# Performance work log

Hardware: AMD Instinct MI355X
Metric: run time of the kernel (lower is better)

Reference implementation:

```python
import jax, jax.numpy as jnp
import numpy as np

N_HEAD = 16


def setup_inputs() -> dict:
    key = jax.random.key(0)
    ks = jax.random.split(key, 4)
    B, S, NX = 2, 2048, 1024
    x = jax.random.normal(ks[0], (B, S, NX), dtype=jnp.float32)
    # additive causal mask: 0 where j <= i, -1e9 where j > i
    causal = jnp.tril(jnp.ones((S, S), dtype=jnp.float32))
    attention_mask = ((1.0 - causal) * -1e9)[None, None, :, :]
    w_attn = jax.random.normal(ks[1], (NX, 3 * NX), dtype=jnp.float32) * 0.02
    b_attn = jnp.zeros((3 * NX,), dtype=jnp.float32)
    w_proj = jax.random.normal(ks[2], (NX, NX), dtype=jnp.float32) * 0.02
    b_proj = jnp.zeros((NX,), dtype=jnp.float32)
    return {"x": x, "attention_mask": attention_mask, "w_attn": w_attn,
            "b_attn": b_attn, "w_proj": w_proj, "b_proj": b_proj}


def reference(x, attention_mask, w_attn, b_attn, w_proj, b_proj):
    B, S, NX = x.shape
    H = N_HEAD
    D = NX // H
    # c_attn (Conv1D): x @ W + b -> [B, S, 3*NX]
    qkv = jnp.einsum('bse,ef->bsf', x, w_attn) + b_attn
    q, k, v = jnp.split(qkv, 3, axis=-1)
    # split heads -> [B, H, S, D]
    q = q.reshape(B, S, H, D).transpose(0, 2, 1, 3)
    k = k.reshape(B, S, H, D).transpose(0, 2, 1, 3)
    v = v.reshape(B, S, H, D).transpose(0, 2, 1, 3)
    # scores [B, H, S, S], scaled by 1/sqrt(head_dim) since scale=True
    w = jnp.einsum('bhqd,bhkd->bhqk', q, k) / jnp.sqrt(jnp.float32(D))
    w = w + attention_mask
    w = jax.nn.softmax(w, axis=-1)
    # attn_dropout is identity in eval / p=0
    a = jnp.einsum('bhqk,bhkd->bhqd', w, v)
    # merge heads -> [B, S, NX]
    a = a.transpose(0, 2, 1, 3).reshape(B, S, NX)
    # c_proj (Conv1D)
    out = jnp.einsum('bse,ef->bsf', a, w_proj) + b_proj
    # resid_dropout identity
    return out
```

## Files before the change

### kernel.cpp

```cpp
#include <hip/hip_runtime.h>
#include <hip/hip_bf16.h>

typedef __bf16 bf16;
typedef __bf16 bf16x8 __attribute__((ext_vector_type(8)));
typedef __bf16 bf16x4 __attribute__((ext_vector_type(4)));
typedef float  f32x4  __attribute__((ext_vector_type(4)));
typedef float  f32x16 __attribute__((ext_vector_type(16)));

#define MFMA16(A,B,C) __builtin_amdgcn_mfma_f32_16x16x32_bf16(A,B,C,0,0,0)
#define MFMA32(A,B,C) __builtin_amdgcn_mfma_f32_32x32x16_bf16(A,B,C,0,0,0)
#define EXP2(x) __builtin_amdgcn_exp2f(x)

static constexpr int SEQ = 2048;
static constexpr int NXC = 1024;
#define QSCALE 0.1803368801111244f

static __device__ inline unsigned packb(float lo, float hi) {
  union { bf16 h[2]; unsigned u; } x;
  x.h[0] = (bf16)lo; x.h[1] = (bf16)hi;
  return x.u;
}
static __device__ inline bf16x8 frag_from_words(unsigned a, unsigned b,
                                                unsigned c, unsigned d) {
  union { unsigned u[4]; bf16x8 v; } x;
  x.u[0] = a; x.u[1] = b; x.u[2] = c; x.u[3] = d;
  return x.v;
}
__device__ __forceinline__ void gload16(const bf16* g, bf16* l) {
  __builtin_amdgcn_global_load_lds(
      (const __attribute__((address_space(1))) void*)g,
      (__attribute__((address_space(3))) void*)l, 16, 0, 0);
}

__global__ __launch_bounds__(256) void f2b_kernel(const float* __restrict__ in,
                                                  bf16* __restrict__ out, int n4) {
  int i = blockIdx.x * blockDim.x + threadIdx.x;
  if (i < n4) {
    float4 v = ((const float4*)in)[i];
    bf16x4 o;
    o[0] = (bf16)v.x; o[1] = (bf16)v.y; o[2] = (bf16)v.z; o[3] = (bf16)v.w;
    ((bf16x4*)out)[i] = o;
  }
}

__global__ __launch_bounds__(256) void tr_f2b(const float* __restrict__ in,
                                              bf16* __restrict__ out, int R, int C) {
  __shared__ bf16 t[64][72];
  const int c0 = blockIdx.x * 64, r0 = blockIdx.y * 64;
  const int tid = threadIdx.x;
  const int lr = tid >> 4, lc = (tid & 15) * 4;
  #pragma unroll
  for (int p = 0; p < 4; ++p) {
    int rr = lr + p * 16;
    float4 v = *(const float4*)&in[(size_t)(r0 + rr) * C + c0 + lc];
    t[lc + 0][rr] = (bf16)v.x; t[lc + 1][rr] = (bf16)v.y;
    t[lc + 2][rr] = (bf16)v.z; t[lc + 3][rr] = (bf16)v.w;
  }
  __syncthreads();
  const int orow = tid >> 3, ocol = (tid & 7) * 8;
  #pragma unroll
  for (int p = 0; p < 2; ++p) {
    int rr = orow + p * 32;
    *(bf16x8*)&out[(size_t)(c0 + rr) * R + r0 + ocol] = *(const bf16x8*)&t[rr][ocol];
  }
}

template<int MODE>
__global__ __launch_bounds__(256) void gemm_bt(
    const bf16* __restrict__ A, const bf16* __restrict__ BT,
    const float* __restrict__ bias,
    bf16* __restrict__ qb, bf16* __restrict__ kb, bf16* __restrict__ vtb,
    float* __restrict__ outf, int K, int N)
{
  __shared__ bf16 As[128 * 32];
  __shared__ bf16 Bs[128 * 32];

  const int tid  = threadIdx.x;
  const int lane = tid & 63;
  const int w    = tid >> 6;
  const int m0   = blockIdx.y * 128;
  const int n0   = blockIdx.x * 128;
  const int wrow = (w >> 1) * 64;
  const int wcol = (w & 1) * 64;
  const int g    = lane >> 4;
  const int c16  = lane & 15;

  f32x4 acc[4][4];
  #pragma unroll
  for (int i = 0; i < 4; ++i)
    #pragma unroll
    for (int j = 0; j < 4; ++j)
      acc[i][j] = f32x4{0.f, 0.f, 0.f, 0.f};

  const bf16* gA = A  + (size_t)(m0 + w * 16 + (lane >> 2)) * K + (lane & 3) * 8;
  const bf16* gB = BT + (size_t)(n0 + w * 16 + (lane >> 2)) * K + (lane & 3) * 8;
  bf16* lA = As + (w * 16) * 32;
  bf16* lB = Bs + (w * 16) * 32;
  const size_t rstep = (size_t)64 * K;

  for (int k0 = 0; k0 < K; k0 += 32) {
    gload16(gA + k0,         lA);
    gload16(gA + k0 + rstep, lA + 64 * 32);
    gload16(gB + k0,         lB);
    gload16(gB + k0 + rstep, lB + 64 * 32);
    __syncthreads();

    bf16x8 af[4], bfr[4];
    #pragma unroll
    for (int i = 0; i < 4; ++i)
      af[i] = *(const bf16x8*)&As[(wrow + i * 16 + c16) * 32 + g * 8];
    #pragma unroll
    for (int j = 0; j < 4; ++j)
      bfr[j] = *(const bf16x8*)&Bs[(wcol + j * 16 + c16) * 32 + g * 8];
    #pragma unroll
    for (int i = 0; i < 4; ++i)
      #pragma unroll
      for (int j = 0; j < 4; ++j)
        acc[i][j] = MFMA16(af[i], bfr[j], acc[i][j]);
    __syncthreads();
  }

  #pragma unroll
  for (int i = 0; i < 4; ++i) {
    #pragma unroll
    for (int j = 0; j < 4; ++j) {
      #pragma unroll
      for (int r = 0; r < 4; ++r) {
        int gm = m0 + wrow + i * 16 + g * 4 + r;
        int gn = n0 + wcol + j * 16 + c16;
        float v = acc[i][j][r] + bias[gn];
        if (MODE == 0) {
          int which = gn >> 10;
          int cc = gn & 1023;
          int hh = cc >> 6, dd = cc & 63;
          int bb = gm >> 11, ss = gm & 2047;
          int bh = bb * 16 + hh;
          if (which == 0)
            qb[((size_t)bh * SEQ + ss) * 64 + dd] = (bf16)(v * QSCALE);
          else if (which == 1)
            kb[((size_t)bh * SEQ + ss) * 64 + dd] = (bf16)v;
          else
            vtb[((size_t)bh * 64 + dd) * SEQ + ss] = (bf16)v;
        } else {
          outf[(size_t)gm * N + gn] = v;
        }
      }
    }
  }
}

__global__ __launch_bounds__(256, 2) void attn7_kernel(
    const bf16* __restrict__ q, const bf16* __restrict__ k,
    const bf16* __restrict__ vt, bf16* __restrict__ aout)
{
  __shared__ bf16 smem[2][8192];

  const int tid  = threadIdx.x;
  const int lane = tid & 63;
  const int w    = tid >> 6;
  const int hi   = lane >> 5;
  const int q_l  = lane & 31;
  const int bid  = blockIdx.x;
  const int bh   = bid & 31;
  const int strip= 15 - (bid >> 5);
  const int qr0  = strip * 128 + w * 32;
  const int qg   = qr0 + q_l;
  const int nt   = 2 * strip + 2;

  bf16x8 qf[4];
  {
    const bf16* qp = q + ((size_t)bh * SEQ + qr0 + q_l) * 64 + hi * 8;
    #pragma unroll
    for (int c = 0; c < 4; ++c) qf[c] = *(const bf16x8*)(qp + c * 16);
  }

  f32x16 Ot0 = (f32x16)0.f, Ot1 = (f32x16)0.f;
  float mrun = -INFINITY, lrun = 0.f;

  const int r1 = tid >> 3;
  const int c1 = (tid & 7) ^ (r1 & 7);
  const bf16* kB = k  + (size_t)bh * SEQ * 64;
  const bf16* vB = vt + (size_t)bh * 64 * SEQ;
  const int sw = q_l & 7;

  auto STAGE = [&](int b, int kv0) {
    bf16* buf = &smem[b][0];
    gload16(kB + (size_t)(kv0 + r1) * 64 + c1 * 8,       buf + w * 512);
    gload16(kB + (size_t)(kv0 + r1 + 32) * 64 + c1 * 8,  buf + 2048 + w * 512);
    gload16(vB + (size_t)r1 * SEQ + kv0 + c1 * 8,        buf + 4096 + w * 512);
    gload16(vB + (size_t)(r1 + 32) * SEQ + kv0 + c1 * 8, buf + 6144 + w * 512);
  };

  auto do_tile = [&](int b, int kv0) {
    const bf16* Kb = &smem[b][0];
    const bf16* Vb = &smem[b][4096];

    bf16x8 kf[8];
    #pragma unroll
    for (int c = 0; c < 4; ++c) {
      int ch = ((2 * c + hi) ^ sw) * 8;
      kf[c]     = *(const bf16x8*)&Kb[q_l * 64 + ch];
      kf[4 + c] = *(const bf16x8*)&Kb[(q_l + 32) * 64 + ch];
    }

    f32x16 st0 = (f32x16)0.f, st1 = (f32x16)0.f;
    __builtin_amdgcn_s_setprio(1);
    #pragma unroll
    for (int c = 0; c < 4; ++c) {
      st0 = MFMA32(kf[c],     qf[c], st0);
      st1 = MFMA32(kf[4 + c], qf[c], st1);
    }
    __builtin_amdgcn_s_setprio(0);

    bf16x8 vf[8];
    #pragma unroll
    for (int t2 = 0; t2 < 2; ++t2)
      #pragma unroll
      for (int h = 0; h < 2; ++h) {
        int ch = ((4 * t2 + 2 * h + hi) ^ sw) * 8;
        vf[t2 * 2 + h]     = *(const bf16x8*)&Vb[q_l * 64 + ch];
        vf[4 + t2 * 2 + h] = *(const bf16x8*)&Vb[(q_l + 32) * 64 + ch];
      }

    if (kv0 + 63 > qr0) {
      #pragma unroll
      for (int r = 0; r < 16; ++r) {
        int kvl = kv0 + (r & 3) + 8 * (r >> 2) + 4 * hi;
        if (kvl > qg)      st0[r] = -1e30f;
        if (kvl + 32 > qg) st1[r] = -1e30f;
      }
    }

    float m8[8];
    #pragma unroll
    for (int r = 0; r < 8; ++r)
      m8[r] = fmaxf(fmaxf(st0[r], st0[r + 8]), fmaxf(st1[r], st1[r + 8]));
    #pragma unroll
    for (int r = 0; r < 4; ++r) m8[r] = fmaxf(m8[r], m8[r + 4]);
    float pmax = fmaxf(fmaxf(m8[0], m8[1]), fmaxf(m8[2], m8[3]));

    float mnew;
    if (__all(pmax <= mrun + 8.f)) {
      mnew = mrun;
    } else {
      float pm = fmaxf(pmax, __shfl_xor(pmax, 32));
      mnew = fmaxf(mrun, pm);
      const float sc = EXP2(mrun - mnew);
      lrun *= sc;
      Ot0 *= sc;
      Ot1 *= sc;
      mrun = mnew;
    }

    #pragma unroll
    for (int r = 0; r < 16; ++r) {
      st0[r] = EXP2(st0[r] - mnew);
      st1[r] = EXP2(st1[r] - mnew);
    }

    float s8[8];
    #pragma unroll
    for (int r = 0; r < 8; ++r)
      s8[r] = (st0[r] + st0[r + 8]) + (st1[r] + st1[r + 8]);
    #pragma unroll
    for (int r = 0; r < 4; ++r) s8[r] += s8[r + 4];
    lrun += (s8[0] + s8[1]) + (s8[2] + s8[3]);

    unsigned pw[16];
    #pragma unroll
    for (int m = 0; m < 8; ++m) {
      pw[m]     = packb(st0[2 * m], st0[2 * m + 1]);
      pw[8 + m] = packb(st1[2 * m], st1[2 * m + 1]);
    }
    __builtin_amdgcn_s_setprio(1);
    #pragma unroll
    for (int t2 = 0; t2 < 2; ++t2) {
      #pragma unroll
      for (int h = 0; h < 2; ++h) {
        auto sa = __builtin_amdgcn_permlane32_swap((int)pw[t2 * 8 + 4 * h + 0],
                                                   (int)pw[t2 * 8 + 4 * h + 2], false, false);
        auto sb = __builtin_amdgcn_permlane32_swap((int)pw[t2 * 8 + 4 * h + 1],
                                                   (int)pw[t2 * 8 + 4 * h + 3], false, false);
        bf16x8 pb = frag_from_words((unsigned)sa[0], (unsigned)sb[0],
                                    (unsigned)sa[1], (unsigned)sb[1]);
        Ot0 = MFMA32(vf[t2 * 2 + h],     pb, Ot0);
        Ot1 = MFMA32(vf[4 + t2 * 2 + h], pb, Ot1);
      }
    }
    __builtin_amdgcn_s_setprio(0);
  };

  STAGE(0, 0);
  asm volatile("s_waitcnt vmcnt(0)" ::: "memory");
  __builtin_amdgcn_s_barrier();

  int cur = 0;
  for (int t = 0; t < nt - 1; ++t) {
    STAGE(cur ^ 1, (t + 1) << 6);
    if ((t << 6) <= qr0 + 31) do_tile(cur, t << 6);
    asm volatile("s_waitcnt vmcnt(0)" ::: "memory");
    __builtin_amdgcn_s_barrier();
    cur ^= 1;
  }
  do_tile(cur, (nt - 1) << 6);


  lrun += __shfl_xor(lrun, 32);
  const float inv = 1.f / lrun;

  __syncthreads();
  bf16* ot = &smem[0][0];
  const int orow = w * 32 + q_l;
  #pragma unroll
  for (int r = 0; r < 16; ++r) {
    int d = (r & 3) + 8 * (r >> 2) + 4 * hi;
    ot[orow * 72 + d]      = (bf16)(Ot0[r] * inv);
    ot[orow * 72 + d + 32] = (bf16)(Ot1[r] * inv);
  }
  __syncthreads();

  const int bb = bh >> 4, hh = bh & 15;
  const int qrow = w * 32 + (lane >> 1), half = lane & 1;
  const bf16* src = ot + qrow * 72 + half * 32;
  bf16* dst = aout + ((size_t)bb * SEQ + strip * 128 + qrow) * NXC + hh * 64 + half * 32;
  #pragma unroll
  for (int e = 0; e < 4; ++e)
    *(bf16x8*)(dst + e * 8) = *(const bf16x8*)(src + e * 8);
}

extern "C" void kernel_launch(void* const* d_in, const int* in_sizes, int n_in,
                              void* d_out, int out_size, void* d_ws, size_t ws_size,
                              hipStream_t stream) {
  const float* x      = (const float*)d_in[0];
  const float* w_attn = (const float*)d_in[2];
  const float* b_attn = (const float*)d_in[3];
  const float* w_proj = (const float*)d_in[4];
  const float* b_proj = (const float*)d_in[5];
  float* out = (float*)d_out;

  char* p = (char*)d_ws;
  bf16* xb   = (bf16*)p; p += (size_t)4194304 * 2;
  bf16* wabT = (bf16*)p; p += (size_t)3145728 * 2;
  bf16* wpbT = (bf16*)p; p += (size_t)1048576 * 2;
  bf16* qb   = (bf16*)p; p += (size_t)4194304 * 2;
  bf16* kb   = (bf16*)p; p += (size_t)4194304 * 2;
  bf16* vtb  = (bf16*)p; p += (size_t)4194304 * 2;
  bf16* ab   = (bf16*)p; p += (size_t)4194304 * 2;

  f2b_kernel<<<4096, 256, 0, stream>>>(x, xb, 1048576);
  tr_f2b<<<dim3(48, 16), 256, 0, stream>>>(w_attn, wabT, 1024, 3072);
  tr_f2b<<<dim3(16, 16), 256, 0, stream>>>(w_proj, wpbT, 1024, 1024);

  gemm_bt<0><<<dim3(24, 32), 256, 0, stream>>>(xb, wabT, b_attn, qb, kb, vtb,
                                               nullptr, 1024, 3072);
  attn7_kernel<<<512, 256, 0, stream>>>(qb, kb, vtb, ab);
  gemm_bt<1><<<dim3(8, 32), 256, 0, stream>>>(ab, wpbT, b_proj, nullptr, nullptr,
                                              nullptr, out, 1024, 1024);
}
```

Baseline: 131.6 us.

## Double-buffer GEMM LDS tiles, swizzle LDS chunks, and remap blocks across XCDs

The QKV and output-projection GEMMs now use two LDS buffers, so the next K-tile's global loads are issued before the current tile's MFMAs and each iteration needs only one barrier. LDS writes and reads use an XOR swizzle on the 8-element chunk index to cut bank conflicts. The 1D grid is remapped so consecutive blocks that land on the same XCD (round-robin over 8) cover neighbouring output tiles, aiming for better L2 reuse. This doubles the GEMM's LDS footprint and assumes the grid size is a multiple of 8.

```diff
diff --git a/kernel.cpp b/kernel.cpp
--- a/kernel.cpp
+++ b/kernel.cpp
@@ -70,16 +70,18 @@
     const bf16* __restrict__ A, const bf16* __restrict__ BT,
     const float* __restrict__ bias,
     bf16* __restrict__ qb, bf16* __restrict__ kb, bf16* __restrict__ vtb,
-    float* __restrict__ outf, int K, int N)
+    float* __restrict__ outf, int K, int N, int nb)
 {
-  __shared__ bf16 As[128 * 32];
-  __shared__ bf16 Bs[128 * 32];
+  __shared__ bf16 As[2][128 * 32];
+  __shared__ bf16 Bs[2][128 * 32];
 
   const int tid  = threadIdx.x;
   const int lane = tid & 63;
   const int w    = tid >> 6;
-  const int m0   = blockIdx.y * 128;
-  const int n0   = blockIdx.x * 128;
+  const int cpx  = gridDim.x >> 3;
+  const int swzb = (blockIdx.x & 7) * cpx + (blockIdx.x >> 3);
+  const int m0   = (swzb / nb) * 128;
+  const int n0   = (swzb % nb) * 128;
   const int wrow = (w >> 1) * 64;
   const int wcol = (w & 1) * 64;
   const int g    = lane >> 4;
@@ -92,32 +94,48 @@
     for (int j = 0; j < 4; ++j)
       acc[i][j] = f32x4{0.f, 0.f, 0.f, 0.f};
 
-  const bf16* gA = A  + (size_t)(m0 + w * 16 + (lane >> 2)) * K + (lane & 3) * 8;
-  const bf16* gB = BT + (size_t)(n0 + w * 16 + (lane >> 2)) * K + (lane & 3) * 8;
-  bf16* lA = As + (w * 16) * 32;
-  bf16* lB = Bs + (w * 16) * 32;
+  const int srow = lane >> 2;
+  const int scol = ((lane & 3) ^ ((lane >> 3) & 3)) * 8;
+  const bf16* gA = A  + (size_t)(m0 + w * 16 + srow) * K + scol;
+  const bf16* gB = BT + (size_t)(n0 + w * 16 + srow) * K + scol;
   const size_t rstep = (size_t)64 * K;
-
-  for (int k0 = 0; k0 < K; k0 += 32) {
+  const int rchunk = (g ^ ((c16 >> 1) & 3)) * 8;
+
+  const int NT = K >> 5;
+
+  auto STAGE = [&](int b, int k0) {
+    bf16* lA = &As[b][w * 512];
+    bf16* lB = &Bs[b][w * 512];
     gload16(gA + k0,         lA);
     gload16(gA + k0 + rstep, lA + 64 * 32);
     gload16(gB + k0,         lB);
     gload16(gB + k0 + rstep, lB + 64 * 32);
-    __syncthreads();
-
+  };
+
+  STAGE(0, 0);
+  __syncthreads();
+
+  int cur = 0;
+  for (int t = 0; t < NT; ++t) {
+    if (t + 1 < NT) STAGE(cur ^ 1, (t + 1) << 5);
+
+    const bf16* pa = &As[cur][0];
+    const bf16* pb = &Bs[cur][0];
     bf16x8 af[4], bfr[4];
     #pragma unroll
     for (int i = 0; i < 4; ++i)
-      af[i] = *(const bf16x8*)&As[(wrow + i * 16 + c16) * 32 + g * 8];
+      af[i] = *(const bf16x8*)&pa[(wrow + i * 16 + c16) * 32 + rchunk];
     #pragma unroll
     for (int j = 0; j < 4; ++j)
-      bfr[j] = *(const bf16x8*)&Bs[(wcol + j * 16 + c16) * 32 + g * 8];
+      bfr[j] = *(const bf16x8*)&pb[(wcol + j * 16 + c16) * 32 + rchunk];
     #pragma unroll
     for (int i = 0; i < 4; ++i)
       #pragma unroll
       for (int j = 0; j < 4; ++j)
         acc[i][j] = MFMA16(af[i], bfr[j], acc[i][j]);
+
     __syncthreads();
+    cur ^= 1;
   }
 
   #pragma unroll
@@ -304,7 +322,6 @@
   }
   do_tile(cur, (nt - 1) << 6);
 
-
   lrun += __shfl_xor(lrun, 32);
   const float inv = 1.f / lrun;
 
@@ -351,9 +368,9 @@
   tr_f2b<<<dim3(48, 16), 256, 0, stream>>>(w_attn, wabT, 1024, 3072);
   tr_f2b<<<dim3(16, 16), 256, 0, stream>>>(w_proj, wpbT, 1024, 1024);
 
-  gemm_bt<0><<<dim3(24, 32), 256, 0, stream>>>(xb, wabT, b_attn, qb, kb, vtb,
-                                               nullptr, 1024, 3072);
+  gemm_bt<0><<<768, 256, 0, stream>>>(xb, wabT, b_attn, qb, kb, vtb,
+                                      nullptr, 1024, 3072, 24);
   attn7_kernel<<<512, 256, 0, stream>>>(qb, kb, vtb, ab);
-  gemm_bt<1><<<dim3(8, 32), 256, 0, stream>>>(ab, wpbT, b_proj, nullptr, nullptr,
-                                              nullptr, out, 1024, 1024);
-}
+  gemm_bt<1><<<256, 256, 0, stream>>>(ab, wpbT, b_proj, nullptr, nullptr,
+                                      nullptr, out, 1024, 1024, 8);
+}
```

New measurement: 119.8 us. 1.1x faster.
